# Kernel tuning notes

Hardware: AMD Instinct MI355X
Metric: run time of the kernel (lower is better)

## Reference

```python
import jax, jax.numpy as jnp
import numpy as np

INDIM = 1024
NHEADS = 16
DK = INDIM // NHEADS  # 64
DV = INDIM // NHEADS  # 64
B, S = 4, 2048


def setup_inputs() -> dict:
    key = jax.random.key(0)
    ks = jax.random.split(key, 5)
    x = jax.random.normal(ks[0], (B, S, INDIM), dtype=jnp.float32)
    std_qk = np.sqrt(2.0 / (INDIM + DK)).astype(np.float32)
    std_v = np.sqrt(2.0 / (INDIM + DV)).astype(np.float32)
    Wq = jax.random.normal(ks[1], (NHEADS * DK, INDIM), dtype=jnp.float32) * std_qk
    Wk = jax.random.normal(ks[2], (NHEADS * DK, INDIM), dtype=jnp.float32) * std_qk
    Wv = jax.random.normal(ks[3], (NHEADS * DV, INDIM), dtype=jnp.float32) * std_v
    # xavier normal for output proj
    std_o = np.sqrt(2.0 / (NHEADS * DV + INDIM)).astype(np.float32)
    Wo = jax.random.normal(ks[4], (INDIM, NHEADS * DV), dtype=jnp.float32) * std_o
    bq = jnp.zeros((NHEADS * DK,), jnp.float32)
    bk = jnp.zeros((NHEADS * DK,), jnp.float32)
    bv = jnp.zeros((NHEADS * DV,), jnp.float32)
    bo = jnp.zeros((INDIM,), jnp.float32)
    return {"x": x, "Wq": Wq, "bq": bq, "Wk": Wk, "bk": bk, "Wv": Wv, "bv": bv, "Wo": Wo, "bo": bo}


def reference(x, Wq, bq, Wk, bk, Wv, bv, Wo, bo):
    b, s, _ = x.shape
    q = (x @ Wq.T + bq).reshape(b, s, NHEADS, DK)
    k = (x @ Wk.T + bk).reshape(b, s, NHEADS, DK)
    v = (x @ Wv.T + bv).reshape(b, s, NHEADS, DV)
    # scores: [b, h, s, z]
    w = jnp.einsum('bshd,bzhd->bhsz', q, k)
    # original divides by sqrt(d_v) (v.size(-1)) when scale=True
    w = w / jnp.sqrt(jnp.float32(DV))
    w = jax.nn.softmax(w, axis=-1)
    vw = jnp.einsum('bhsz,bzhd->bshd', w, v)  # [b, s, h, dv]
    vw = vw.reshape(b, s, NHEADS * DV)
    out = vw @ Wo.T + bo
    return out
```

## Files before the change

kernel.cpp:

```cpp
#include <hip/hip_runtime.h>
#include <hip/hip_bf16.h>
#include <cstdint>
#include <cstddef>

#define NHEADS 16
#define HDIM   64
#define SEQ    2048
#define BATCH  4
#define IND    1024
#define MTOT   (BATCH*SEQ)

typedef __attribute__((ext_vector_type(8))) short bf16x8;
typedef __attribute__((ext_vector_type(4))) float f32x4;
typedef __attribute__((ext_vector_type(16))) float f32x16;
typedef __attribute__((ext_vector_type(2))) int i32x2;
typedef __attribute__((ext_vector_type(4))) unsigned u32x4;

__device__ __forceinline__ unsigned short f2b(float f) {
  unsigned u = __builtin_bit_cast(unsigned, f);
  u += 0x7FFFu + ((u >> 16) & 1u);
  return (unsigned short)(u >> 16);
}
__device__ __forceinline__ unsigned cvt2(float lo, float hi) {
  float2 t; t.x = lo; t.y = hi;
  __hip_bfloat162 h = __float22bfloat162_rn(t);
  const unsigned short ulo = __bfloat16_as_ushort(h.x);
  const unsigned short uhi = __bfloat16_as_ushort(h.y);
  return (unsigned)ulo | ((unsigned)uhi << 16);
}
__device__ __forceinline__ float m3(float a, float b, float c) {
  return fmaxf(fmaxf(a, b), c);
}

__device__ __forceinline__ void gload_lds16(const void* g, void* l) {
  __builtin_amdgcn_global_load_lds(
      (const __attribute__((address_space(1))) void*)g,
      (__attribute__((address_space(3))) void*)l, 16, 0, 0);
}

__global__ void cvt_kernel(const float* __restrict__ src,
                           unsigned short* __restrict__ dst, int n4) {
  int i = blockIdx.x * blockDim.x + threadIdx.x;
  const int stride = gridDim.x * blockDim.x;
  for (; i < n4; i += stride) {
    const float4 v = reinterpret_cast<const float4*>(src)[i];
    ushort4 o;
    o.x = f2b(v.x); o.y = f2b(v.y); o.z = f2b(v.z); o.w = f2b(v.w);
    reinterpret_cast<ushort4*>(dst)[i] = o;
  }
}

__global__ void cvtw_kernel(const float* __restrict__ w0, const float* __restrict__ w1,
                            const float* __restrict__ w2, const float* __restrict__ w3,
                            unsigned short* __restrict__ o0, unsigned short* __restrict__ o1,
                            unsigned short* __restrict__ o2, unsigned short* __restrict__ o3,
                            int n4) {
  const int z = blockIdx.y;
  const float* src = (z == 0) ? w0 : (z == 1) ? w1 : (z == 2) ? w2 : w3;
  unsigned short* dst = (z == 0) ? o0 : (z == 1) ? o1 : (z == 2) ? o2 : o3;
  int i = blockIdx.x * blockDim.x + threadIdx.x;
  const int stride = gridDim.x * blockDim.x;
  for (; i < n4; i += stride) {
    const float4 v = reinterpret_cast<const float4*>(src)[i];
    ushort4 o;
    o.x = f2b(v.x); o.y = f2b(v.y); o.z = f2b(v.z); o.w = f2b(v.w);
    reinterpret_cast<ushort4*>(dst)[i] = o;
  }
}

template<int EPI>
__device__ __forceinline__ void gemm_core(
    const unsigned short* __restrict__ A,
    const unsigned short* __restrict__ Bw,
    const float* __restrict__ bias,
    void* __restrict__ Cout, float scale)
{
  __shared__ alignas(16) unsigned short As[2][4096];
  __shared__ alignas(16) unsigned short Bs[2][4096];
  const int tid = threadIdx.x;
  const int wv = tid >> 6, lane = tid & 63, g = lane >> 4, li = lane & 15;
  const int wr = (wv >> 1) * 64, wc = (wv & 1) * 64;
  const int m0 = blockIdx.x * 128, n0 = blockIdx.y * 128;

  auto stage = [&](int buf, int kt) {
    const int k0 = kt * 32;
#pragma unroll
    for (int rnd = 0; rnd < 2; ++rnd) {
      const int f = (tid + rnd * 256) * 8;
      const int row = f >> 5, col = f & 31;
      gload_lds16(&A[(size_t)(m0 + row) * IND + k0 + col], &As[buf][f]);
      gload_lds16(&Bw[(size_t)(n0 + row) * IND + k0 + col], &Bs[buf][f]);
    }
  };

  f32x4 acc[4][4] = {};
  stage(0, 0);
  for (int kt = 0; kt < 32; ++kt) {
    __syncthreads();
    if (kt + 1 < 32) stage((kt + 1) & 1, kt + 1);
    const int buf = kt & 1;
    bf16x8 af[4], bfr[4];
#pragma unroll
    for (int i = 0; i < 4; ++i)
      af[i] = *(const bf16x8*)&As[buf][(wr + i * 16 + li) * 32 + g * 8];
#pragma unroll
    for (int i = 0; i < 4; ++i)
      bfr[i] = *(const bf16x8*)&Bs[buf][(wc + i * 16 + li) * 32 + g * 8];
#pragma unroll
    for (int mi = 0; mi < 4; ++mi)
#pragma unroll
      for (int ni = 0; ni < 4; ++ni)
        acc[mi][ni] = __builtin_amdgcn_mfma_f32_16x16x32_bf16(
            af[mi], bfr[ni], acc[mi][ni], 0, 0, 0);
  }

#pragma unroll
  for (int ni = 0; ni < 4; ++ni) {
    const int col = n0 + wc + ni * 16 + li;
    const float bz = bias[col];
#pragma unroll
    for (int mi = 0; mi < 4; ++mi) {
#pragma unroll
      for (int r = 0; r < 4; ++r) {
        const int row = m0 + wr + mi * 16 + g * 4 + r;
        float v = acc[mi][ni][r] + bz;
        if (EPI == 0) {
          v *= scale;
          const int h = col >> 6, d = col & 63;
          const int b = row >> 11, s = row & 2047;
          ((unsigned short*)Cout)[(((size_t)(b * NHEADS + h)) * SEQ + s) * HDIM + d] = f2b(v);
        } else if (EPI == 2) {
          const int h = col >> 6, d = col & 63;
          const int b = row >> 11, s = row & 2047;
          ((unsigned short*)Cout)[(((size_t)(b * NHEADS + h)) * HDIM + d) * SEQ + s] = f2b(v);
        } else {
          ((float*)Cout)[(size_t)row * IND + col] = v;
        }
      }
    }
  }
}

__global__ __launch_bounds__(256, 2)
void gemm_qkv_kernel(const unsigned short* __restrict__ xb,
                     const unsigned short* __restrict__ Wq,
                     const unsigned short* __restrict__ Wk,
                     const unsigned short* __restrict__ Wv,
                     const float* __restrict__ bq,
                     const float* __restrict__ bk,
                     const float* __restrict__ bv,
                     unsigned short* __restrict__ Qo,
                     unsigned short* __restrict__ Ko,
                     unsigned short* __restrict__ Vto)
{
  const int z = blockIdx.z;
  if (z == 2) {
    gemm_core<2>(xb, Wv, bv, Vto, 1.0f);
  } else {
    const unsigned short* Bw = (z == 0) ? Wq : Wk;
    const float* bias = (z == 0) ? bq : bk;
    unsigned short* out = (z == 0) ? Qo : Ko;
    const float scale = (z == 0) ? 0.18033688011111772f : 1.0f;
    gemm_core<0>(xb, Bw, bias, out, scale);
  }
}

__global__ __launch_bounds__(256, 2)
void gemm_o_kernel(const unsigned short* __restrict__ Ab,
                   const unsigned short* __restrict__ Wo,
                   const float* __restrict__ bo,
                   float* __restrict__ out)
{
  gemm_core<1>(Ab, Wo, bo, out, 1.0f);
}

__global__ __launch_bounds__(256, 4)
void attn_kernel(const unsigned short* __restrict__ Q,
                 const unsigned short* __restrict__ K,
                 const unsigned short* __restrict__ Vt,
                 unsigned short* __restrict__ O)
{
  __shared__ alignas(16) unsigned short Kb[2][64 * 64];
  __shared__ alignas(16) unsigned short Vb[2][64 * 64];

  const int tid = threadIdx.x;
  const int wv = tid >> 6, lane = tid & 63;
  const int r31 = lane & 31, hi = lane >> 5;

  const unsigned flat = blockIdx.x;
  const unsigned wg = (flat & 7) * 128 + (flat >> 3);
  const int qblk = wg & 15;
  const int bh = wg >> 4;

  const size_t hbase = (size_t)bh * (SEQ * HDIM);
  const unsigned short* Qh = Q + hbase;
  const unsigned short* Kh = K + hbase;
  const unsigned short* Vh = Vt + hbase;
  const int q0 = qblk * 128 + wv * 32;

  bf16x8 qf[4];
#pragma unroll
  for (int kc = 0; kc < 4; ++kc)
    qf[kc] = *(const bf16x8*)&Qh[(size_t)(q0 + r31) * HDIM + kc * 16 + hi * 8];

  f32x16 accO[2] = {};
  float m_run = -INFINITY, l_run = 0.0f;

  auto stage = [&](int buf, int kv) {
    const int k0 = kv * 64;
#pragma unroll
    for (int rnd = 0; rnd < 2; ++rnd) {
      const int c = tid + rnd * 256;
      const int row = c >> 3, pch = c & 7;
      const int ch = pch ^ (row & 7);
      gload_lds16(&Kh[(size_t)(k0 + row) * HDIM + ch * 8], &Kb[buf][c * 8]);
      gload_lds16(&Vh[(size_t)row * SEQ + k0 + ch * 8], &Vb[buf][c * 8]);
    }
  };

  stage(0, 0);

  for (int kv = 0; kv < SEQ / 64; ++kv) {
    __syncthreads();
    if (kv + 1 < SEQ / 64) stage((kv + 1) & 1, kv + 1);
    const int buf = kv & 1;

    f32x16 s0 = {}, s1 = {};
#pragma unroll
    for (int kc = 0; kc < 4; ++kc) {
      const int pch = (kc * 2 + hi) ^ (r31 & 7);
      const int base = r31 * 64 + pch * 8;
      const bf16x8 kf0 = *(const bf16x8*)&Kb[buf][base];
      s0 = __builtin_amdgcn_mfma_f32_32x32x16_bf16(kf0, qf[kc], s0, 0, 0, 0);
      const bf16x8 kf1 = *(const bf16x8*)&Kb[buf][base + 2048];
      s1 = __builtin_amdgcn_mfma_f32_32x32x16_bf16(kf1, qf[kc], s1, 0, 0, 0);
    }

    float t0 = m3(s0[0], s0[1], s0[2]),   t1 = m3(s0[3], s0[4], s0[5]);
    float t2 = m3(s0[6], s0[7], s0[8]),   t3 = m3(s0[9], s0[10], s0[11]);
    float t4 = m3(s0[12], s0[13], s0[14]);
    float u0 = m3(t0, t1, s0[15]),        u1 = fmaxf(t2, fmaxf(t3, t4));
    float t5 = m3(s1[0], s1[1], s1[2]),   t6 = m3(s1[3], s1[4], s1[5]);
    float t7 = m3(s1[6], s1[7], s1[8]),   t8 = m3(s1[9], s1[10], s1[11]);
    float t9 = m3(s1[12], s1[13], s1[14]);
    float u2 = m3(t5, t6, s1[15]),        u3 = fmaxf(t7, fmaxf(t8, t9));
    float pmax = m3(fmaxf(u0, u1), u2, u3);
    pmax = fmaxf(pmax, __shfl_xor(pmax, 32));

    if (!__all(pmax - m_run <= 8.0f)) {
      const float mn = fmaxf(m_run, pmax);
      const float al = exp2f(m_run - mn);
      l_run *= al;
#pragma unroll
      for (int f = 0; f < 2; ++f)
#pragma unroll
        for (int r = 0; r < 16; ++r) accO[f][r] *= al;
      m_run = mn;
    }

    unsigned pk[16];
    float rs = 0.0f;
#pragma unroll
    for (int i = 0; i < 8; ++i) {
      const float ea = exp2f(s0[2 * i] - m_run);
      const float eb = exp2f(s0[2 * i + 1] - m_run);
      rs += ea + eb;
      pk[i] = cvt2(ea, eb);
    }
#pragma unroll
    for (int i = 0; i < 8; ++i) {
      const float ea = exp2f(s1[2 * i] - m_run);
      const float eb = exp2f(s1[2 * i + 1] - m_run);
      rs += ea + eb;
      pk[8 + i] = cvt2(ea, eb);
    }
    rs += __shfl_xor(rs, 32);
    l_run += rs;

    bf16x8 pf[4];
#pragma unroll
    for (int kc2 = 0; kc2 < 4; ++kc2) {
      const int bs = kc2 * 4;
      const i32x2 rA = __builtin_amdgcn_permlane32_swap(
          (int)pk[bs + 0], (int)pk[bs + 2], false, false);
      const i32x2 rB = __builtin_amdgcn_permlane32_swap(
          (int)pk[bs + 1], (int)pk[bs + 3], false, false);
      u32x4 u;
      u[0] = (unsigned)rA[0];
      u[1] = (unsigned)rB[0];
      u[2] = (unsigned)rA[1];
      u[3] = (unsigned)rB[1];
      pf[kc2] = __builtin_bit_cast(bf16x8, u);
    }

#pragma unroll
    for (int kc2 = 0; kc2 < 4; ++kc2) {
      const int pch = (kc2 * 2 + hi) ^ (r31 & 7);
      const int vbase = r31 * 64 + pch * 8;
      const bf16x8 vf0 = *(const bf16x8*)&Vb[buf][vbase];
      accO[0] = __builtin_amdgcn_mfma_f32_32x32x16_bf16(vf0, pf[kc2], accO[0], 0, 0, 0);
      const bf16x8 vf1 = *(const bf16x8*)&Vb[buf][vbase + 2048];
      accO[1] = __builtin_amdgcn_mfma_f32_32x32x16_bf16(vf1, pf[kc2], accO[1], 0, 0, 0);
    }
  }

  const int b = bh >> 4, h = bh & 15;
  const float inv = 1.0f / l_run;
  const int qrow = q0 + r31;
  unsigned short* obase = (unsigned short*)&O[((size_t)(b * SEQ + qrow)) * IND + h * HDIM];
#pragma unroll
  for (int f = 0; f < 2; ++f) {
#pragma unroll
    for (int half = 0; half < 4; ++half) {
      uint2 w;
      w.x = cvt2(accO[f][half * 4 + 0] * inv, accO[f][half * 4 + 1] * inv);
      w.y = cvt2(accO[f][half * 4 + 2] * inv, accO[f][half * 4 + 3] * inv);
      *(uint2*)&obase[32 * f + 8 * half + 4 * hi] = w;
    }
  }
}

extern "C" void kernel_launch(void* const* d_in, const int* in_sizes, int n_in,
                              void* d_out, int out_size, void* d_ws, size_t ws_size,
                              hipStream_t stream) {
  const float* x  = (const float*)d_in[0];
  const float* Wq = (const float*)d_in[1];
  const float* bq = (const float*)d_in[2];
  const float* Wk = (const float*)d_in[3];
  const float* bk = (const float*)d_in[4];
  const float* Wv = (const float*)d_in[5];
  const float* bv = (const float*)d_in[6];
  const float* Wo = (const float*)d_in[7];
  const float* bo = (const float*)d_in[8];

  char* ws = (char*)d_ws;
  constexpr size_t SZ_XB = (size_t)MTOT * IND * 2;
  constexpr size_t SZ_W  = (size_t)IND * IND * 2;
  unsigned short* xb   = (unsigned short*)(ws);
  unsigned short* Wqb  = (unsigned short*)(ws + SZ_XB);
  unsigned short* Wkb  = (unsigned short*)(ws + SZ_XB + SZ_W);
  unsigned short* Wvb  = (unsigned short*)(ws + SZ_XB + 2 * SZ_W);
  unsigned short* Wob  = (unsigned short*)(ws + SZ_XB + 3 * SZ_W);
  unsigned short* Qb   = (unsigned short*)(ws + SZ_XB + 4 * SZ_W);
  unsigned short* Kbuf = (unsigned short*)(ws + 2 * SZ_XB + 4 * SZ_W);
  unsigned short* Vtb  = (unsigned short*)(ws + 3 * SZ_XB + 4 * SZ_W);
  unsigned short* AOb  = (unsigned short*)(ws + 4 * SZ_XB + 4 * SZ_W);

  cvt_kernel<<<2048, 256, 0, stream>>>(x, xb, (MTOT * IND) / 4);
  cvtw_kernel<<<dim3(512, 4), 256, 0, stream>>>(Wq, Wk, Wv, Wo,
                                                Wqb, Wkb, Wvb, Wob, (IND * IND) / 4);

  gemm_qkv_kernel<<<dim3(MTOT / 128, IND / 128, 3), 256, 0, stream>>>(
      xb, Wqb, Wkb, Wvb, bq, bk, bv, Qb, Kbuf, Vtb);

  attn_kernel<<<dim3(16 * BATCH * NHEADS), 256, 0, stream>>>(Qb, Kbuf, Vtb, AOb);

  gemm_o_kernel<<<dim3(MTOT / 128, IND / 128), 256, 0, stream>>>(
      AOb, Wob, bo, (float*)d_out);
}
```

Baseline: 238.3 us.

## Use fp16 P·V with MFMA row-sum and native exp2 in attention

V is now stored as fp16 and the softmax probabilities are packed with the hardware round-toward-zero fp16 convert, so the P·V MFMA runs in f16 instead of bf16 and the manual round-to-nearest bf16 conversion goes away. The per-row softmax denominator is no longer summed with VALU adds and a cross-lane shuffle. An extra MFMA against a ones vector accumulates it instead. exp2f is replaced by the native amdgcn exp2 builtin. This trades VALU work in the softmax for one more MFMA per k-chunk and slightly different rounding and range behaviour in fp16.

Result: faster. 207.3 us (-13.0%).

```diff
diff --git a/kernel.cpp b/kernel.cpp
--- a/kernel.cpp
+++ b/kernel.cpp
@@ -11,10 +11,18 @@
 #define MTOT   (BATCH*SEQ)
 
 typedef __attribute__((ext_vector_type(8))) short bf16x8;
+typedef __attribute__((ext_vector_type(8))) _Float16 f16x8;
+typedef __attribute__((ext_vector_type(2))) _Float16 f16x2;
 typedef __attribute__((ext_vector_type(4))) float f32x4;
 typedef __attribute__((ext_vector_type(16))) float f32x16;
 typedef __attribute__((ext_vector_type(2))) int i32x2;
 typedef __attribute__((ext_vector_type(4))) unsigned u32x4;
+
+#if __has_builtin(__builtin_amdgcn_exp2f)
+#define EXP2(x) __builtin_amdgcn_exp2f(x)
+#else
+#define EXP2(x) exp2f(x)
+#endif
 
 __device__ __forceinline__ unsigned short f2b(float f) {
   unsigned u = __builtin_bit_cast(unsigned, f);
@@ -132,7 +140,7 @@
         } else if (EPI == 2) {
           const int h = col >> 6, d = col & 63;
           const int b = row >> 11, s = row & 2047;
-          ((unsigned short*)Cout)[(((size_t)(b * NHEADS + h)) * HDIM + d) * SEQ + s] = f2b(v);
+          ((_Float16*)Cout)[(((size_t)(b * NHEADS + h)) * HDIM + d) * SEQ + s] = (_Float16)v;
         } else {
           ((float*)Cout)[(size_t)row * IND + col] = v;
         }
@@ -203,8 +211,16 @@
   for (int kc = 0; kc < 4; ++kc)
     qf[kc] = *(const bf16x8*)&Qh[(size_t)(q0 + r31) * HDIM + kc * 16 + hi * 8];
 
+  f16x8 onesA;
+  {
+    const _Float16 ov = (r31 == 0) ? (_Float16)1.0f : (_Float16)0.0f;
+#pragma unroll
+    for (int j = 0; j < 8; ++j) onesA[j] = ov;
+  }
+
   f32x16 accO[2] = {};
-  float m_run = -INFINITY, l_run = 0.0f;
+  f32x16 accL = {};
+  float m_run = -INFINITY;
 
   auto stage = [&](int buf, int kv) {
     const int k0 = kv * 64;
@@ -249,35 +265,30 @@
 
     if (!__all(pmax - m_run <= 8.0f)) {
       const float mn = fmaxf(m_run, pmax);
-      const float al = exp2f(m_run - mn);
-      l_run *= al;
+      const float al = EXP2(m_run - mn);
 #pragma unroll
       for (int f = 0; f < 2; ++f)
 #pragma unroll
         for (int r = 0; r < 16; ++r) accO[f][r] *= al;
+      accL[0] *= al;
       m_run = mn;
     }
 
     unsigned pk[16];
-    float rs = 0.0f;
 #pragma unroll
     for (int i = 0; i < 8; ++i) {
-      const float ea = exp2f(s0[2 * i] - m_run);
-      const float eb = exp2f(s0[2 * i + 1] - m_run);
-      rs += ea + eb;
-      pk[i] = cvt2(ea, eb);
+      const float ea = EXP2(s0[2 * i] - m_run);
+      const float eb = EXP2(s0[2 * i + 1] - m_run);
+      pk[i] = __builtin_bit_cast(unsigned, __builtin_amdgcn_cvt_pkrtz(ea, eb));
     }
 #pragma unroll
     for (int i = 0; i < 8; ++i) {
-      const float ea = exp2f(s1[2 * i] - m_run);
-      const float eb = exp2f(s1[2 * i + 1] - m_run);
-      rs += ea + eb;
-      pk[8 + i] = cvt2(ea, eb);
-    }
-    rs += __shfl_xor(rs, 32);
-    l_run += rs;
-
-    bf16x8 pf[4];
+      const float ea = EXP2(s1[2 * i] - m_run);
+      const float eb = EXP2(s1[2 * i + 1] - m_run);
+      pk[8 + i] = __builtin_bit_cast(unsigned, __builtin_amdgcn_cvt_pkrtz(ea, eb));
+    }
+
+    f16x8 pf[4];
 #pragma unroll
     for (int kc2 = 0; kc2 < 4; ++kc2) {
       const int bs = kc2 * 4;
@@ -290,22 +301,26 @@
       u[1] = (unsigned)rB[0];
       u[2] = (unsigned)rA[1];
       u[3] = (unsigned)rB[1];
-      pf[kc2] = __builtin_bit_cast(bf16x8, u);
+      pf[kc2] = __builtin_bit_cast(f16x8, u);
     }
 
 #pragma unroll
     for (int kc2 = 0; kc2 < 4; ++kc2) {
       const int pch = (kc2 * 2 + hi) ^ (r31 & 7);
       const int vbase = r31 * 64 + pch * 8;
-      const bf16x8 vf0 = *(const bf16x8*)&Vb[buf][vbase];
-      accO[0] = __builtin_amdgcn_mfma_f32_32x32x16_bf16(vf0, pf[kc2], accO[0], 0, 0, 0);
-      const bf16x8 vf1 = *(const bf16x8*)&Vb[buf][vbase + 2048];
-      accO[1] = __builtin_amdgcn_mfma_f32_32x32x16_bf16(vf1, pf[kc2], accO[1], 0, 0, 0);
-    }
-  }
+      const f16x8 vf0 = *(const f16x8*)&Vb[buf][vbase];
+      accO[0] = __builtin_amdgcn_mfma_f32_32x32x16_f16(vf0, pf[kc2], accO[0], 0, 0, 0);
+      const f16x8 vf1 = *(const f16x8*)&Vb[buf][vbase + 2048];
+      accO[1] = __builtin_amdgcn_mfma_f32_32x32x16_f16(vf1, pf[kc2], accO[1], 0, 0, 0);
+      accL = __builtin_amdgcn_mfma_f32_32x32x16_f16(onesA, pf[kc2], accL, 0, 0, 0);
+    }
+  }
+
+  float lv = accL[0];
+  lv += __shfl_xor(lv, 32);
 
   const int b = bh >> 4, h = bh & 15;
-  const float inv = 1.0f / l_run;
+  const float inv = 1.0f / lv;
   const int qrow = q0 + r31;
   unsigned short* obase = (unsigned short*)&O[((size_t)(b * SEQ + qrow)) * IND + h * HDIM];
 #pragma unroll
```
